# Performance work log

Hardware: AMD Instinct MI355X
Metric: run time of the kernel (lower is better)

Reference implementation:

```python
import jax, jax.numpy as jnp
import numpy as np

B, L, D = 256, 512, 512

def setup_inputs() -> dict:
    key = jax.random.key(0)
    k1, k2, k3, k4, k5 = jax.random.split(key, 5)
    scale = 1.0 / np.sqrt(D)  # keep logits in a sane range
    return {
        "text_features": jax.random.normal(k1, (B, L, D), dtype=jnp.float32),
        "image_features": jax.random.normal(k2, (B, D), dtype=jnp.float32),
        "W_ML": jax.random.normal(k3, (D, D), dtype=jnp.float32) * scale,
        "W_MV": jax.random.normal(k4, (D, D), dtype=jnp.float32) * scale,
        "tau": jnp.ones((1,), dtype=jnp.float32),
        "padding_mask": jax.random.randint(k5, (B, L), 0, 2).astype(bool),
    }

def reference(text_features, image_features, W_ML, W_MV, tau, padding_mask):
    b, l, _ = text_features.shape
    tau_c = jnp.clip(tau, 0.001)  # [1]
    valid = ~padding_mask  # [B,L] True where token is real
    # Linear(bias=False): y = x @ W.T
    text_proj = jnp.einsum('bld,ed->ble', text_features, W_ML)   # [B,L,D]
    image_proj = jnp.einsum('bd,ed->be', image_features, W_MV)   # [B,D]
    neg_inf = jnp.float32(-jnp.inf)
    # positive scores: own image vs own text tokens
    s_iji = jnp.einsum('bd,bld->bl', image_proj, text_proj) / tau_c  # [B,L]
    # all-images-vs-text denominator: s_kji[i,l,k] = <text[i,l], image[k]>
    s_kji = jnp.einsum('ild,kd->ilk', text_proj, image_proj) / tau_c  # [B,L,B]
    mask_kj = valid.T[None, :, :]  # [1,L,B] -> valid[k,l] per (i,l,k)
    s_kji = jnp.where(mask_kj, s_kji, neg_inf)
    denom_log = jax.nn.logsumexp(s_kji, axis=2)  # [B,L]
    # cross-batch text negatives: s_iok[i,k,l] = <image[i], text[k,l]>
    s_iok = jnp.einsum('id,kld->ikl', image_proj, text_proj) / tau_c  # [B,B,L]
    mask_ko = valid[None, :, :]  # [1,B,L]
    mask_neq = ~jnp.eye(b, dtype=bool)[:, :, None]  # exclude k == i
    s_iok_f = jnp.where(mask_ko & mask_neq, s_iok, neg_inf).reshape(b, -1)
    cross_log = jax.nn.logsumexp(s_iok_f, axis=1)  # [B]
    neg_log = jnp.logaddexp(s_iji, cross_log[:, None])  # [B,L]
    denom_log = jnp.where(valid, denom_log, 0.0)
    neg_log = jnp.where(valid, neg_log, 0.0)
    f1 = denom_log - s_iji
    f2 = neg_log - s_iji
    loss_mat = 0.5 * (f1 + f2)
    n_valid = jnp.sum(valid)
    loss = jnp.sum(jnp.where(valid, loss_mat, 0.0)) / n_valid
    return loss
```

## Files before the change

### kernel.cpp

```cpp
#include <hip/hip_runtime.h>
#include <math.h>


#define B_ 256
#define L_ 512
#define D_ 512
#define ROWS (B_ * L_)
#define NT (ROWS / 64)
#define NEG_INF (-INFINITY)

typedef __attribute__((ext_vector_type(8))) short s8_t;
typedef __attribute__((ext_vector_type(4))) float f4_t;
typedef __attribute__((ext_vector_type(2))) float f2_t;
typedef __attribute__((ext_vector_type(4))) unsigned short us4_t;

typedef __attribute__((address_space(3))) unsigned int lds_u32;
typedef const __attribute__((address_space(1))) unsigned int glb_u32;

__device__ inline unsigned short f2bf(float x) {
    unsigned int u = __float_as_uint(x);
    u += 0x7FFFu + ((u >> 16) & 1u);
    return (unsigned short)(u >> 16);
}

__global__ __launch_bounds__(256) void ip_kernel(const float* __restrict__ img,
                                                 const float* __restrict__ Wmv,
                                                 float* __restrict__ ip) {
    int kt = blockIdx.x >> 3, et = blockIdx.x & 7;
    __shared__ float Ast[32][36];
    __shared__ float Bst[32][72];
    int tid = threadIdx.x;
    int ty = tid >> 4;
    int tx = tid & 15;
    float acc[2][4] = {};
    int sr = tid >> 3, sc = (tid & 7) * 4;
    for (int d0 = 0; d0 < D_; d0 += 32) {
        f4_t a = *(const f4_t*)(img + (size_t)(kt * 32 + sr) * D_ + d0 + sc);
        f4_t b0 = *(const f4_t*)(Wmv + (size_t)(et * 64 + sr) * D_ + d0 + sc);
        f4_t b1 = *(const f4_t*)(Wmv + (size_t)(et * 64 + sr + 32) * D_ + d0 + sc);
        __syncthreads();
#pragma unroll
        for (int m = 0; m < 4; m++) {
            Ast[sc + m][sr] = a[m];
            Bst[sc + m][sr] = b0[m];
            Bst[sc + m][sr + 32] = b1[m];
        }
        __syncthreads();
#pragma unroll 4
        for (int d = 0; d < 32; d++) {
            f2_t a2 = *(const f2_t*)&Ast[d][ty * 2];
            f4_t b4 = *(const f4_t*)&Bst[d][tx * 4];
#pragma unroll
            for (int i = 0; i < 2; i++)
#pragma unroll
                for (int j = 0; j < 4; j++) acc[i][j] = fmaf(a2[i], b4[j], acc[i][j]);
        }
    }
#pragma unroll
    for (int i = 0; i < 2; i++) {
        f4_t o; o[0] = acc[i][0]; o[1] = acc[i][1]; o[2] = acc[i][2]; o[3] = acc[i][3];
        *(f4_t*)(ip + (size_t)(kt * 32 + ty * 2 + i) * D_ + et * 64 + tx * 4) = o;
    }
}

__global__ __launch_bounds__(256) void c_kernel(const float* __restrict__ ip,
                                                const float* __restrict__ Wml,
                                                const float* __restrict__ tau,
                                                unsigned short* __restrict__ Cb2) {
    int kt = blockIdx.x >> 3, dt = blockIdx.x & 7;
    __shared__ float Ast[32][36];
    __shared__ float Bst[32][72];
    int tid = threadIdx.x;
    int ty = tid >> 4;
    int tx = tid & 15;
    float acc[2][4] = {};
    int sr = tid >> 3, sc = (tid & 7) * 4;
    int br = tid >> 4, bc = (tid & 15) * 4;
    for (int e0 = 0; e0 < D_; e0 += 32) {
        f4_t a = *(const f4_t*)(ip + (size_t)(kt * 32 + sr) * D_ + e0 + sc);
        f4_t b0 = *(const f4_t*)(Wml + (size_t)(e0 + br) * D_ + dt * 64 + bc);
        f4_t b1 = *(const f4_t*)(Wml + (size_t)(e0 + br + 16) * D_ + dt * 64 + bc);
        __syncthreads();
#pragma unroll
        for (int m = 0; m < 4; m++) Ast[sc + m][sr] = a[m];
        *(f4_t*)&Bst[br][bc] = b0;
        *(f4_t*)&Bst[br + 16][bc] = b1;
        __syncthreads();
#pragma unroll 4
        for (int e = 0; e < 32; e++) {
            f2_t a2 = *(const f2_t*)&Ast[e][ty * 2];
            f4_t b4 = *(const f4_t*)&Bst[e][tx * 4];
#pragma unroll
            for (int i = 0; i < 2; i++)
#pragma unroll
                for (int j = 0; j < 4; j++) acc[i][j] = fmaf(a2[i], b4[j], acc[i][j]);
        }
    }
    float it = 1.0f / fmaxf(tau[0], 0.001f);
#pragma unroll
    for (int i = 0; i < 2; i++) {
        us4_t o;
#pragma unroll
        for (int j = 0; j < 4; j++) o[j] = f2bf(acc[i][j] * it);
        int n = kt * 32 + ty * 2 + i;
        int kk0 = dt * 64 + tx * 4;
        *(us4_t*)(Cb2 + (size_t)((kk0 >> 3) * 256 + n) * 8 + (kk0 & 7)) = o;
    }
}

__global__ __launch_bounds__(256) void mask_kernel(const int* __restrict__ pad,
                                                   unsigned long long* __restrict__ mbits) {
    int l = blockIdx.x;
    int w = threadIdx.x >> 6;
    int j = threadIdx.x & 63;
    unsigned long long bal = __ballot(pad[(w * 64 + j) * L_ + l] == 0);
    if (j == 0) mbits[l * 4 + w] = bal;
}

#define ACC(mt, nt, r) ((mt) ? acc1[nt][r] : acc0[nt][r])

#define MERGE_XOR(m, s, msk) do {                                        \
        float mo_ = __shfl_xor(m, msk);                                  \
        float so_ = __shfl_xor(s, msk);                                  \
        float M_ = fmaxf(m, mo_);                                        \
        s = (M_ > NEG_INF) ? (s * __expf(m - M_) + so_ * __expf(mo_ - M_)) : 0.f; \
        m = M_;                                                          \
    } while (0)

__global__ __launch_bounds__(256, 4) void gemm_mfma_kernel(
    const float* __restrict__ text, const unsigned short* __restrict__ Cb2,
    const unsigned long long* __restrict__ mbits,
    float* __restrict__ denom, float* __restrict__ siji,
    float* __restrict__ crossM, float* __restrict__ crossS) {
    __shared__ __align__(16) unsigned char smem[32768];

    const int tile = blockIdx.x;
    const int row0 = tile * 64;
    const int bIdx = row0 >> 9;
    const int l0 = row0 & 511;
    const int tid = threadIdx.x;
    const int wave = tid >> 6;
    const int lane = tid & 63;
    const int qd = lane >> 4;
    const int mm = lane & 15;
    const int wr = wave >> 1;
    const int wc = wave & 1;

    f4_t acc0[8], acc1[8];
#pragma unroll
    for (int nt = 0; nt < 8; nt++)
#pragma unroll
        for (int r = 0; r < 4; r++) { acc0[nt][r] = 0.f; acc1[nt][r] = 0.f; }

    const float* aRow = text + (size_t)(row0 + wr * 32 + mm) * D_ + qd * 8;

    f4_t ar0[4], ar1[4];
#define LOAD_A(dst, t) do { \
        dst[0] = *(const f4_t*)(aRow + (t) * 32); \
        dst[1] = *(const f4_t*)(aRow + (t) * 32 + 4); \
        dst[2] = *(const f4_t*)(aRow + 16 * D_ + (t) * 32); \
        dst[3] = *(const f4_t*)(aRow + 16 * D_ + (t) * 32 + 4); \
    } while (0)

#define STAGE(buf, t) do { \
        const unsigned char* gsrc_ = (const unsigned char*)Cb2 + (size_t)(t) * 16384 + wave * 1024 + lane * 16; \
        unsigned char* ldst_ = smem + (buf) * 16384 + wave * 1024; \
        _Pragma("unroll") \
        for (int i_ = 0; i_ < 4; i_++) \
            __builtin_amdgcn_global_load_lds((glb_u32*)(gsrc_ + i_ * 4096), \
                                             (lds_u32*)(ldst_ + i_ * 4096), 16, 0, 0); \
    } while (0)

#define CVT(arc, aa0, aa1) do { \
        _Pragma("unroll") \
        for (int j_ = 0; j_ < 4; j_++) { \
            aa0[j_] = (short)f2bf(arc[0][j_]); aa0[j_ + 4] = (short)f2bf(arc[1][j_]); \
            aa1[j_] = (short)f2bf(arc[2][j_]); aa1[j_ + 4] = (short)f2bf(arc[3][j_]); \
        } \
    } while (0)

#define MFMA8(rb, aa0, aa1) do { \
        const unsigned short* bbase_ = \
            (const unsigned short*)(smem + (rb) * 16384) + qd * 2048 + (wc * 128 + mm) * 8; \
        _Pragma("unroll") \
        for (int nt_ = 0; nt_ < 8; nt_++) { \
            s8_t bf_ = *(const s8_t*)(bbase_ + nt_ * 128); \
            acc0[nt_] = __builtin_amdgcn_mfma_f32_16x16x32_bf16(aa0, bf_, acc0[nt_], 0, 0, 0); \
            acc1[nt_] = __builtin_amdgcn_mfma_f32_16x16x32_bf16(aa1, bf_, acc1[nt_], 0, 0, 0); \
        } \
    } while (0)

#define ITER(tt, rb, sb, arc) do { \
        STAGE(sb, (tt) + 1); \
        __builtin_amdgcn_sched_barrier(0); \
        s8_t aa0_, aa1_; \
        CVT(arc, aa0_, aa1_); \
        LOAD_A(arc, (tt) + 2); \
        __builtin_amdgcn_sched_barrier(0); \
        MFMA8(rb, aa0_, aa1_); \
        asm volatile("s_waitcnt vmcnt(4)" ::: "memory"); \
        __builtin_amdgcn_s_barrier(); \
    } while (0)

    STAGE(0, 0);
    __builtin_amdgcn_sched_barrier(0);
    LOAD_A(ar0, 0);
    LOAD_A(ar1, 1);
    __builtin_amdgcn_sched_barrier(0);
    asm volatile("s_waitcnt vmcnt(8)" ::: "memory");
    __builtin_amdgcn_s_barrier();

#pragma unroll 1
    for (int t = 0; t < 14; t += 2) {
        ITER(t,     0, 1, ar0);
        ITER(t + 1, 1, 0, ar1);
    }
    {
        STAGE(1, 15);
        __builtin_amdgcn_sched_barrier(0);
        s8_t aa0_, aa1_;
        CVT(ar0, aa0_, aa1_);
        MFMA8(0, aa0_, aa1_);
        asm volatile("s_waitcnt vmcnt(0)" ::: "memory");
        __builtin_amdgcn_s_barrier();
    }
    {
        s8_t aa0_, aa1_;
        CVT(ar1, aa0_, aa1_);
        MFMA8(1, aa0_, aa1_);
    }
    __syncthreads();

    float* fp  = (float*)smem;
    float* pmp = fp;
    float* psp = fp + 128;
    float* cmp = fp + 256;
    float* csp = fp + 768;

    const int mw = bIdx >> 6, mb = bIdx & 63;

    float radj[2][4];
#pragma unroll
    for (int mt = 0; mt < 2; mt++)
#pragma unroll
        for (int r = 0; r < 4; r++) {
            int l = l0 + wr * 32 + mt * 16 + qd * 4 + r;
            radj[mt][r] = ((mbits[l * 4 + mw] >> mb) & 1ULL) ? 0.f : NEG_INF;
        }

#pragma unroll
    for (int nt = 0; nt < 8; nt++) {
        float m = NEG_INF;
#pragma unroll
        for (int mt = 0; mt < 2; mt++)
#pragma unroll
            for (int r = 0; r < 4; r++) m = fmaxf(m, ACC(mt, nt, r) + radj[mt][r]);
        float s = 0.f;
        if (m > NEG_INF) {
#pragma unroll
            for (int mt = 0; mt < 2; mt++)
#pragma unroll
                for (int r = 0; r < 4; r++) s += __expf(ACC(mt, nt, r) + radj[mt][r] - m);
        }
        MERGE_XOR(m, s, 16);
        MERGE_XOR(m, s, 32);
        if (qd == 0) {
            int col = wc * 128 + nt * 16 + mm;
            cmp[wr * 256 + col] = m;
            csp[wr * 256 + col] = s;
        }
    }

#pragma unroll
    for (int mt = 0; mt < 2; mt++)
#pragma unroll
        for (int r = 0; r < 4; r++) {
            int rl = wr * 32 + mt * 16 + qd * 4 + r;
            int l = l0 + rl;
            unsigned long long w0 = mbits[l * 4 + wc * 2] >> mm;
            unsigned long long w1 = mbits[l * 4 + wc * 2 + 1] >> mm;
            float v[8];
#pragma unroll
            for (int nt = 0; nt < 4; nt++) {
                v[nt]     = ACC(mt, nt, r)     + (((w0 >> (nt * 16)) & 1ULL) ? 0.f : NEG_INF);
                v[nt + 4] = ((mt) ? acc1[nt + 4][r] : acc0[nt + 4][r])
                            + (((w1 >> (nt * 16)) & 1ULL) ? 0.f : NEG_INF);
            }
            float m = NEG_INF;
#pragma unroll
            for (int nt = 0; nt < 8; nt++) m = fmaxf(m, v[nt]);
            float s = 0.f;
            if (m > NEG_INF) {
#pragma unroll
                for (int nt = 0; nt < 8; nt++) s += __expf(v[nt] - m);
            }
            MERGE_XOR(m, s, 1);
            MERGE_XOR(m, s, 2);
            MERGE_XOR(m, s, 4);
            MERGE_XOR(m, s, 8);
            if (mm == 0) { pmp[wc * 64 + rl] = m; psp[wc * 64 + rl] = s; }
        }

#pragma unroll
    for (int nt = 0; nt < 8; nt++)
        if (wc == (bIdx >> 7) && mm == (bIdx & 15) && nt == ((bIdx >> 4) & 7)) {
#pragma unroll
            for (int mt = 0; mt < 2; mt++)
#pragma unroll
                for (int r = 0; r < 4; r++)
                    siji[row0 + wr * 32 + mt * 16 + qd * 4 + r] = ACC(mt, nt, r);
        }

    __syncthreads();

    if (tid < 64) {
        float m0 = pmp[tid], m1 = pmp[64 + tid];
        float s0 = psp[tid], s1 = psp[64 + tid];
        float M = fmaxf(m0, m1);
        float dl = NEG_INF;
        if (M > NEG_INF) dl = M + __logf(s0 * __expf(m0 - M) + s1 * __expf(m1 - M));
        denom[row0 + tid] = dl;
    }
    {
        int col = tid;
        float m0 = cmp[col], m1 = cmp[256 + col];
        float s0 = csp[col], s1 = csp[256 + col];
        float M = fmaxf(m0, m1);
        float s = (M > NEG_INF) ? (s0 * __expf(m0 - M) + s1 * __expf(m1 - M)) : 0.f;
        if (col == bIdx) { M = NEG_INF; s = 0.f; }
        crossM[(size_t)col * NT + tile] = M;
        crossS[(size_t)col * NT + tile] = s;
    }
#undef LOAD_A
#undef STAGE
#undef CVT
#undef MFMA8
#undef ITER
}

__global__ __launch_bounds__(256) void cross_combine_kernel(const float* __restrict__ crossM,
                                                            const float* __restrict__ crossS,
                                                            float* __restrict__ crossLog) {
    int i = blockIdx.x;
    int tid = threadIdx.x;
    float m = NEG_INF, s = 0.f;
    for (int e = 0; e < NT / 256; e++) {
        int t = e * 256 + tid;
        float m2 = crossM[(size_t)i * NT + t];
        float s2 = crossS[(size_t)i * NT + t];
        if (m2 > NEG_INF) {
            if (m == NEG_INF) { m = m2; s = s2; }
            else {
                float M = fmaxf(m, m2);
                s = s * expf(m - M) + s2 * expf(m2 - M);
                m = M;
            }
        }
    }
    __shared__ float sm[256], ss[256];
    sm[tid] = m; ss[tid] = s;
    __syncthreads();
    for (int off = 128; off > 0; off >>= 1) {
        if (tid < off) {
            float m1 = sm[tid], s1 = ss[tid];
            float m2 = sm[tid + off], s2 = ss[tid + off];
            float M = fmaxf(m1, m2);
            float sv;
            if (M == NEG_INF) sv = 0.f;
            else sv = s1 * expf(m1 - M) + s2 * expf(m2 - M);
            sm[tid] = M; ss[tid] = sv;
        }
        __syncthreads();
    }
    if (tid == 0) crossLog[i] = (sm[0] == NEG_INF) ? NEG_INF : sm[0] + logf(ss[0]);
}

__global__ __launch_bounds__(256) void loss_partial_kernel(
    const int* __restrict__ pad, const float* __restrict__ denom,
    const float* __restrict__ siji, const float* __restrict__ crossLog,
    float* __restrict__ psum, float* __restrict__ pcnt) {
    int tid = threadIdx.x;
    int idx = blockIdx.x * 256 + tid;
    float term = 0.f, cnt = 0.f;
    if (pad[idx] == 0) {
        float dl = denom[idx], sv = siji[idx], cl = crossLog[idx >> 9];
        float M = fmaxf(sv, cl);
        float neg = M + log1pf(expf(-fabsf(sv - cl)));
        term = 0.5f * (dl + neg) - sv;
        cnt = 1.f;
    }
    __shared__ float bs[256], bc[256];
    bs[tid] = term; bc[tid] = cnt;
    __syncthreads();
    for (int off = 128; off > 0; off >>= 1) {
        if (tid < off) { bs[tid] += bs[tid + off]; bc[tid] += bc[tid + off]; }
        __syncthreads();
    }
    if (tid == 0) { psum[blockIdx.x] = bs[0]; pcnt[blockIdx.x] = bc[0]; }
}

__global__ __launch_bounds__(256) void final_kernel(const float* __restrict__ psum,
                                                    const float* __restrict__ pcnt,
                                                    float* __restrict__ out) {
    int tid = threadIdx.x;
    __shared__ float bs[256], bc[256];
    bs[tid] = psum[tid] + psum[tid + 256];
    bc[tid] = pcnt[tid] + pcnt[tid + 256];
    __syncthreads();
    for (int off = 128; off > 0; off >>= 1) {
        if (tid < off) { bs[tid] += bs[tid + off]; bc[tid] += bc[tid + off]; }
        __syncthreads();
    }
    if (tid == 0) out[0] = bs[0] / bc[0];
}

extern "C" void kernel_launch(void* const* d_in, const int* in_sizes, int n_in,
                              void* d_out, int out_size, void* d_ws, size_t ws_size,
                              hipStream_t stream) {
    (void)in_sizes; (void)n_in; (void)out_size; (void)ws_size;
    const float* text = (const float*)d_in[0];
    const float* img  = (const float*)d_in[1];
    const float* Wml  = (const float*)d_in[2];
    const float* Wmv  = (const float*)d_in[3];
    const float* tau  = (const float*)d_in[4];
    const int* pad    = (const int*)d_in[5];
    float* out = (float*)d_out;

    float* ws = (float*)d_ws;
    float* ip       = ws;
    unsigned short* Cb2 = (unsigned short*)(ws + 131072);
    unsigned long long* mbits = (unsigned long long*)(ws + 262144);
    float* denom    = ws + 266240;
    float* siji     = ws + 397312;
    float* crossM   = ws + 528384;
    float* crossS   = ws + 1052672;
    float* crossLog = ws + 1576960;
    float* psum     = ws + 1577216;
    float* pcnt     = ws + 1577728;

    hipLaunchKernelGGL(ip_kernel,   dim3(64),  dim3(256), 0, stream, img, Wmv, ip);
    hipLaunchKernelGGL(c_kernel,    dim3(64),  dim3(256), 0, stream, ip, Wml, tau, Cb2);
    hipLaunchKernelGGL(mask_kernel, dim3(L_),  dim3(256), 0, stream, pad, mbits);
    hipLaunchKernelGGL(gemm_mfma_kernel, dim3(NT), dim3(256), 0, stream,
                       text, Cb2, mbits, denom, siji, crossM, crossS);
    hipLaunchKernelGGL(cross_combine_kernel, dim3(B_), dim3(256), 0, stream,
                       crossM, crossS, crossLog);
    hipLaunchKernelGGL(loss_partial_kernel, dim3(ROWS / 256), dim3(256), 0, stream,
                       pad, denom, siji, crossLog, psum, pcnt);
    hipLaunchKernelGGL(final_kernel, dim3(1), dim3(256), 0, stream, psum, pcnt, out);
}
```

Measured before the change: 463.0 us.

## Triple-buffer B tiles in LDS to prefetch two steps ahead

```diff
diff --git a/kernel.cpp b/kernel.cpp
--- a/kernel.cpp
+++ b/kernel.cpp
@@ -127,12 +127,12 @@
         m = M_;                                                          \
     } while (0)
 
-__global__ __launch_bounds__(256, 4) void gemm_mfma_kernel(
+__global__ __launch_bounds__(256, 3) void gemm_mfma_kernel(
     const float* __restrict__ text, const unsigned short* __restrict__ Cb2,
     const unsigned long long* __restrict__ mbits,
     float* __restrict__ denom, float* __restrict__ siji,
     float* __restrict__ crossM, float* __restrict__ crossS) {
-    __shared__ __align__(16) unsigned char smem[32768];
+    __shared__ __align__(16) unsigned char smem[49152];
 
     const int tile = blockIdx.x;
     const int row0 = tile * 64;
@@ -162,9 +162,9 @@
         dst[3] = *(const f4_t*)(aRow + 16 * D_ + (t) * 32 + 4); \
     } while (0)
 
-#define STAGE(buf, t) do { \
+#define STAGE_P(bufp, t) do { \
         const unsigned char* gsrc_ = (const unsigned char*)Cb2 + (size_t)(t) * 16384 + wave * 1024 + lane * 16; \
-        unsigned char* ldst_ = smem + (buf) * 16384 + wave * 1024; \
+        unsigned char* ldst_ = (bufp) + wave * 1024; \
         _Pragma("unroll") \
         for (int i_ = 0; i_ < 4; i_++) \
             __builtin_amdgcn_global_load_lds((glb_u32*)(gsrc_ + i_ * 4096), \
@@ -179,9 +179,9 @@
         } \
     } while (0)
 
-#define MFMA8(rb, aa0, aa1) do { \
+#define MFMA8_P(bufp, aa0, aa1) do { \
         const unsigned short* bbase_ = \
-            (const unsigned short*)(smem + (rb) * 16384) + qd * 2048 + (wc * 128 + mm) * 8; \
+            (const unsigned short*)(bufp) + qd * 2048 + (wc * 128 + mm) * 8; \
         _Pragma("unroll") \
         for (int nt_ = 0; nt_ < 8; nt_++) { \
             s8_t bf_ = *(const s8_t*)(bbase_ + nt_ * 128); \
@@ -190,44 +190,49 @@
         } \
     } while (0)
 
-#define ITER(tt, rb, sb, arc) do { \
-        STAGE(sb, (tt) + 1); \
+#define ITER(tc, bR, bS, arX) do { \
+        STAGE_P(bS, (tc) + 2); \
         __builtin_amdgcn_sched_barrier(0); \
         s8_t aa0_, aa1_; \
-        CVT(arc, aa0_, aa1_); \
-        LOAD_A(arc, (tt) + 2); \
-        __builtin_amdgcn_sched_barrier(0); \
-        MFMA8(rb, aa0_, aa1_); \
-        asm volatile("s_waitcnt vmcnt(4)" ::: "memory"); \
+        CVT(arX, aa0_, aa1_); \
+        LOAD_A(arX, (tc) + 2); \
+        MFMA8_P(bR, aa0_, aa1_); \
+        asm volatile("s_waitcnt vmcnt(12)" ::: "memory"); \
         __builtin_amdgcn_s_barrier(); \
     } while (0)
 
-    STAGE(0, 0);
+    unsigned char* bA = smem;
+    unsigned char* bB = smem + 16384;
+    unsigned char* bC = smem + 32768;
+
+    STAGE_P(bA, 0);
     __builtin_amdgcn_sched_barrier(0);
     LOAD_A(ar0, 0);
+    __builtin_amdgcn_sched_barrier(0);
+    STAGE_P(bB, 1);
+    __builtin_amdgcn_sched_barrier(0);
     LOAD_A(ar1, 1);
     __builtin_amdgcn_sched_barrier(0);
-    asm volatile("s_waitcnt vmcnt(8)" ::: "memory");
+    asm volatile("s_waitcnt vmcnt(12)" ::: "memory");
     __builtin_amdgcn_s_barrier();
 
 #pragma unroll 1
     for (int t = 0; t < 14; t += 2) {
-        ITER(t,     0, 1, ar0);
-        ITER(t + 1, 1, 0, ar1);
+        ITER(t,     bA, bC, ar0);
+        ITER(t + 1, bB, bA, ar1);
+        unsigned char* tmp = bA; bA = bC; bC = bB; bB = tmp;
     }
     {
-        STAGE(1, 15);
-        __builtin_amdgcn_sched_barrier(0);
         s8_t aa0_, aa1_;
         CVT(ar0, aa0_, aa1_);
-        MFMA8(0, aa0_, aa1_);
-        asm volatile("s_waitcnt vmcnt(0)" ::: "memory");
+        MFMA8_P(bA, aa0_, aa1_);
+        asm volatile("s_waitcnt vmcnt(4)" ::: "memory");
         __builtin_amdgcn_s_barrier();
     }
     {
         s8_t aa0_, aa1_;
         CVT(ar1, aa0_, aa1_);
-        MFMA8(1, aa0_, aa1_);
+        MFMA8_P(bB, aa0_, aa1_);
     }
     __syncthreads();
 
@@ -332,9 +337,9 @@
         crossS[(size_t)col * NT + tile] = s;
     }
 #undef LOAD_A
-#undef STAGE
+#undef STAGE_P
 #undef CVT
-#undef MFMA8
+#undef MFMA8_P
 #undef ITER
 }
 
```

New measurement: 465.7 us. About the same (+0.6%).
